# Performance work log

Measured on AMD Instinct MI355X. Metric: run time of the kernel, lower is better.

Reference implementation:

```python
import jax, jax.numpy as jnp
import numpy as np

EMBED = 2048
N_EXPERTS = 64
TOP_K = 8


def setup_inputs() -> dict:
    key = jax.random.key(0)
    k_x, k_w, k_b = jax.random.split(key, 3)
    inputs = jax.random.normal(k_x, (8, 4096, EMBED), dtype=jnp.float32)
    # nn.Linear(embed_size, num_experts): weight [E, D], bias [E]
    bound = 1.0 / np.sqrt(EMBED)
    W = jax.random.uniform(k_w, (N_EXPERTS, EMBED), dtype=jnp.float32, minval=-bound, maxval=bound)
    b = jax.random.uniform(k_b, (N_EXPERTS,), dtype=jnp.float32, minval=-bound, maxval=bound)
    return {"inputs": inputs, "W": W, "b": b}


def reference(inputs, W, b):
    # scores: [B, S, E]
    scores = jnp.einsum("bsd,ed->bse", inputs, W) + b
    topk_scores, indices = jax.lax.top_k(scores, TOP_K)  # [B,S,K]
    # scatter topk_scores into a zero mask (non-selected slots stay 0.0)
    onehot = jax.nn.one_hot(indices, N_EXPERTS, dtype=scores.dtype)  # [B,S,K,E]
    mask = jnp.einsum("bske,bsk->bse", onehot, topk_scores)
    router_output = jax.nn.softmax(mask, axis=-1)
    return (router_output, indices)
```

## Files before the change

kernel.cpp:

```cpp
#include <hip/hip_runtime.h>
#include <math.h>

#define N_TOKENS 32768
#define EMBED    2048
#define NEXP     64
#define TOPK     8
#define BM       64
#define BK       64
#define NCH      (EMBED / BK)
#define SCS      65
#define THRESH   1e-4f
#define WELEMS   (NEXP * EMBED)
#define FIXGRID  1024

typedef __attribute__((ext_vector_type(8)))  short short8;
typedef __attribute__((ext_vector_type(16))) float f32x16;
typedef __attribute__((ext_vector_type(4)))  unsigned int uint4v;

__device__ __forceinline__ unsigned pkbf(float a, float b) {
  unsigned r;
  asm("v_cvt_pk_bf16_f32 %0, %1, %2" : "=v"(r) : "v"(a), "v"(b));
  return r;
}

__device__ __forceinline__ void cvt8(float4 fa, float4 fb, short8* h8, short8* l8) {
  const unsigned h0 = pkbf(fa.x, fa.y), h1 = pkbf(fa.z, fa.w);
  const unsigned h2 = pkbf(fb.x, fb.y), h3 = pkbf(fb.z, fb.w);
  const float l0 = fa.x - __uint_as_float(h0 << 16);
  const float l1 = fa.y - __uint_as_float(h0 & 0xFFFF0000u);
  const float l2 = fa.z - __uint_as_float(h1 << 16);
  const float l3 = fa.w - __uint_as_float(h1 & 0xFFFF0000u);
  const float l4 = fb.x - __uint_as_float(h2 << 16);
  const float l5 = fb.y - __uint_as_float(h2 & 0xFFFF0000u);
  const float l6 = fb.z - __uint_as_float(h3 << 16);
  const float l7 = fb.w - __uint_as_float(h3 & 0xFFFF0000u);
  const uint4v H = {h0, h1, h2, h3};
  const uint4v L = {pkbf(l0, l1), pkbf(l2, l3), pkbf(l4, l5), pkbf(l6, l7)};
  *h8 = __builtin_bit_cast(short8, H);
  *l8 = __builtin_bit_cast(short8, L);
}

__global__ void split_w(const float* __restrict__ W, short* __restrict__ wh,
                        short* __restrict__ wl, int* __restrict__ gcnt) {
  if (blockIdx.x == 0 && threadIdx.x == 0) *gcnt = 0;
  const int T = blockIdx.x * 256 + threadIdx.x;
  const int n = T >> 8, kg8 = T & 255;
  const float4* W4 = (const float4*)W;
  float4 a = W4[n * 512 + kg8 * 2];
  float4 b = W4[n * 512 + kg8 * 2 + 1];
  short8 h, l;
  cvt8(a, b, &h, &l);
  *(short8*)&wh[(kg8 * 64 + n) * 8] = h;
  *(short8*)&wl[(kg8 * 64 + n) * 8] = l;
}

__global__ __launch_bounds__(256, 2)
void router_kernel(const float* __restrict__ x, const short* __restrict__ wh,
                   const short* __restrict__ wl, const float* __restrict__ bias,
                   int* __restrict__ gcnt, int* __restrict__ glist,
                   float* __restrict__ out) {
  __shared__ float4 lx[3][1024];
  float* sc = (float*)&lx[0][0];

  const int tid  = threadIdx.x;
  const int t0   = blockIdx.x * BM;
  const int lane = tid & 63;
  const int w    = tid >> 6;
  const int half = lane >> 5;
  const int r5   = lane & 31;
  const int tw   = (w & 1) * 32;
  const int ew   = (w >> 1) * 32;

  const float4* x4g = (const float4*)x;
  const short8* Bh  = (const short8*)wh;
  const short8* Bl  = (const short8*)wl;
  const int boff = half * 64 + ew + r5;

  const int row16 = tid >> 4;
  const int s4    = tid & 15;
  const int c4sw  = s4 ^ row16;
  const int wbase = (tid & 192);

  const float4* gbase = x4g + (size_t)(t0 + row16) * (EMBED / 4) + c4sw;

#pragma unroll
  for (int i = 0; i < 4; ++i)
    __builtin_amdgcn_global_load_lds((const void*)(gbase + (size_t)16 * i * (EMBED / 4)),
                                     (void*)&lx[0][i * 256 + wbase], 16, 0, 0);
#pragma unroll
  for (int i = 0; i < 4; ++i)
    __builtin_amdgcn_global_load_lds((const void*)(gbase + (size_t)16 * i * (EMBED / 4) + 16),
                                     (void*)&lx[1][i * 256 + wbase], 16, 0, 0);

  const int arow  = tw + r5;
  const int am    = arow & 15;
  const int abase = (arow >> 4) * 256 + am * 16;

  f32x16 acc;
#pragma unroll
  for (int i = 0; i < 16; ++i) acc[i] = 0.f;

  int bc = 0, bp = 2;
  for (int ch = 0; ch < NCH; ++ch) {
    if (ch + 1 < NCH) asm volatile("s_waitcnt vmcnt(4)" ::: "memory");
    else              asm volatile("s_waitcnt vmcnt(0)" ::: "memory");
    __builtin_amdgcn_s_barrier();
    __builtin_amdgcn_sched_barrier(0);

    short8 bh[4], bl[4];
#pragma unroll
    for (int s = 0; s < 4; ++s) {
      const int bi = (ch * 4 + s) * 128 + boff;
      bh[s] = Bh[bi]; bl[s] = Bl[bi];
    }
    __builtin_amdgcn_sched_barrier(0);

    if (ch + 2 < NCH) {
#pragma unroll
      for (int i = 0; i < 4; ++i)
        __builtin_amdgcn_global_load_lds(
            (const void*)(gbase + (size_t)16 * i * (EMBED / 4) + (ch + 2) * 16),
            (void*)&lx[bp][i * 256 + wbase], 16, 0, 0);
    }

#pragma unroll
    for (int s = 0; s < 4; ++s) {
      const int c0 = s * 4 + half * 2;
      float4 fa = lx[bc][abase + (c0 ^ am)];
      float4 fb = lx[bc][abase + ((c0 + 1) ^ am)];
      short8 ah, al;
      cvt8(fa, fb, &ah, &al);
      acc = __builtin_amdgcn_mfma_f32_32x32x16_bf16(ah, bh[s], acc, 0, 0, 0);
      acc = __builtin_amdgcn_mfma_f32_32x32x16_bf16(ah, bl[s], acc, 0, 0, 0);
      acc = __builtin_amdgcn_mfma_f32_32x32x16_bf16(al, bh[s], acc, 0, 0, 0);
    }
    bc = (bc == 2) ? 0 : bc + 1;
    bp = (bp == 2) ? 0 : bp + 1;
  }

  __syncthreads();

#pragma unroll
  for (int reg = 0; reg < 16; ++reg) {
    const int row = (reg & 3) + 8 * (reg >> 2) + 4 * half;
    sc[(tw + row) * SCS + ew + r5] = acc[reg];
  }
  __syncthreads();

  float* rout = out;
  float* iout = out + (size_t)N_TOKENS * NEXP;
  const float bias_l = bias[lane];

  for (int tb = 0; tb < 4; ++tb) {
    const int tbase = w * 16 + tb * 4;
    float orig[4]; unsigned cur[4];
#pragma unroll
    for (int i = 0; i < 4; ++i) {
      orig[i] = sc[(tbase + i) * SCS + lane] + bias_l;
      unsigned b = __float_as_uint(orig[i]);
      unsigned u = b ^ (((unsigned)((int)b >> 31)) | 0x80000000u);
      cur[i] = (u & 0xFFFFFFC0u) | (63u - (unsigned)lane);
    }
    float m[4], Z[4], ming[4], prev[4], morig[4];
    int myidx[4]; bool sel[4];
#pragma unroll
    for (int i = 0; i < 4; ++i) { sel[i] = false; morig[i] = 0.f; myidx[i] = 0; ming[i] = 1e30f; }

#pragma unroll
    for (int r = 0; r < 9; ++r) {
      unsigned v[4];
#pragma unroll
      for (int i = 0; i < 4; ++i) v[i] = cur[i];
#pragma unroll
      for (int s2 = 1; s2 < 64; s2 <<= 1) {
#pragma unroll
        for (int i = 0; i < 4; ++i) {
          unsigned o = (unsigned)__shfl_xor((int)v[i], s2);
          v[i] = v[i] > o ? v[i] : o;
        }
      }
#pragma unroll
      for (int i = 0; i < 4; ++i) {
        unsigned vb = (v[i] & 0x80000000u) ? (v[i] ^ 0x80000000u) : ~v[i];
        float fv = __uint_as_float(vb);
        if (r == 0) { m[i] = fmaxf(fv, 0.f); Z[i] = 56.f * expf(-m[i]) + expf(fv - m[i]); }
        else {
          ming[i] = fminf(ming[i], prev[i] - fv);
          if (r < 8) Z[i] += expf(fv - m[i]);
        }
        prev[i] = fv;
        if (r < 8) {
          if (lane == r) myidx[i] = 63 - (int)(v[i] & 63u);
          if (cur[i] == v[i]) { sel[i] = true; morig[i] = orig[i]; cur[i] = 0u; }
        }
      }
    }
#pragma unroll
    for (int i = 0; i < 4; ++i) {
      const int t = tbase + i;
      if (ming[i] < THRESH) {
        if (lane == 0) { int p = atomicAdd(gcnt, 1); glist[p] = t0 + t; }
      } else {
        const float p = expf(morig[i] - m[i]) / Z[i];
        rout[(size_t)(t0 + t) * NEXP + lane] = p;
        if (lane < TOPK) iout[(size_t)(t0 + t) * TOPK + lane] = (float)myidx[i];
      }
    }
  }
}

__global__ __launch_bounds__(256, 4)
void fixup_kernel(const float* __restrict__ x, const float* __restrict__ Wf,
                  const float* __restrict__ bias, const int* __restrict__ gcnt,
                  const int* __restrict__ glist, float* __restrict__ out) {
  __shared__ float4 xsh[512];
  __shared__ double sco[NEXP];
  const int tid  = threadIdx.x;
  const int lane = tid & 63;
  const int w    = tid >> 6;
  float* rout = out;
  float* iout = out + (size_t)N_TOKENS * NEXP;
  const int cnt = *gcnt;

  for (int j = blockIdx.x; j < cnt; j += FIXGRID) {
    const int tok = glist[j];
    const float4* xr = (const float4*)x + (size_t)tok * 512;
    xsh[tid] = xr[tid];
    xsh[tid + 256] = xr[tid + 256];
    __syncthreads();

    for (int i = 0; i < 16; ++i) {
      const int e = w * 16 + i;
      const float4* wr = (const float4*)Wf + (size_t)e * 512;
      double a = 0.0;
#pragma unroll
      for (int q = 0; q < 8; ++q) {
        float4 wv = wr[q * 64 + lane];
        float4 xv = xsh[q * 64 + lane];
        a = fma((double)xv.x, (double)wv.x, a);
        a = fma((double)xv.y, (double)wv.y, a);
        a = fma((double)xv.z, (double)wv.z, a);
        a = fma((double)xv.w, (double)wv.w, a);
      }
#pragma unroll
      for (int s2 = 1; s2 < 64; s2 <<= 1) a += __shfl_xor(a, s2);
      if (lane == 0) sco[e] = a + (double)bias[e];
    }
    __syncthreads();

    if (w == 0) {
      const double orig = sco[lane];
      double curd = orig, vals[8];
      int myidx = 0; double mym = 0.0;
#pragma unroll
      for (int r = 0; r < 8; ++r) {
        double v = curd; int id = lane;
#pragma unroll
        for (int s2 = 1; s2 < 64; s2 <<= 1) {
          const double ov = __shfl_xor(v, s2);
          const int    oi = __shfl_xor(id, s2);
          if (ov > v || (ov == v && oi < id)) { v = ov; id = oi; }
        }
        vals[r] = v;
        if (lane == r)  myidx = id;
        if (lane == id) { mym = orig; curd = -1e300; }
      }
      const double md = fmax(vals[0], 0.0);
      double Zd = 56.0 * exp(-md);
#pragma unroll
      for (int r = 0; r < 8; ++r) Zd += exp(vals[r] - md);
      const double p = exp(mym - md) / Zd;
      rout[(size_t)tok * NEXP + lane] = (float)p;
      if (lane < TOPK) iout[(size_t)tok * TOPK + lane] = (float)myidx;
    }
    __syncthreads();
  }
}

extern "C" void kernel_launch(void* const* d_in, const int* in_sizes, int n_in,
                              void* d_out, int out_size, void* d_ws, size_t ws_size,
                              hipStream_t stream) {
  const float* x = (const float*)d_in[0];
  const float* W = (const float*)d_in[1];
  const float* b = (const float*)d_in[2];
  short* wh = (short*)d_ws;
  short* wl = wh + WELEMS;
  int* gcnt  = (int*)(wl + WELEMS);
  int* glist = gcnt + 4;

  split_w<<<64, 256, 0, stream>>>(W, wh, wl, gcnt);
  router_kernel<<<N_TOKENS / BM, 256, 0, stream>>>(x, wh, wl, b, gcnt, glist,
                                                   (float*)d_out);
  fixup_kernel<<<FIXGRID, 256, 0, stream>>>(x, W, b, gcnt, glist, (float*)d_out);
}
```

Baseline: 465.9 us.

## Deepen x prefetch to four LDS buffers and software-pipeline weight loads

Moves from a 3-deep to a 4-deep LDS ring for x chunks, so x tiles are prefetched three chunks ahead instead of two. The global loads of the bf16 weight fragments for the next chunk are now issued a full iteration ahead into alternating register sets, so they overlap with the current chunk's MFMAs. The loop is unrolled by two and the last chunks are peeled, with explicit vmcnt waits. This adds LDS use, which may reduce occupancy, and more registers, and it relies on precise vmcnt accounting. It also removes an unused sel flag.

Measured after the change: 467.4 us. Within noise of the previous version (+0.3%).

```diff
diff --git a/kernel.cpp b/kernel.cpp
--- a/kernel.cpp
+++ b/kernel.cpp
@@ -59,7 +59,7 @@
                    const short* __restrict__ wl, const float* __restrict__ bias,
                    int* __restrict__ gcnt, int* __restrict__ glist,
                    float* __restrict__ out) {
-  __shared__ float4 lx[3][1024];
+  __shared__ float4 lx[4][1024];
   float* sc = (float*)&lx[0][0];
 
   const int tid  = threadIdx.x;
@@ -83,15 +83,6 @@
 
   const float4* gbase = x4g + (size_t)(t0 + row16) * (EMBED / 4) + c4sw;
 
-#pragma unroll
-  for (int i = 0; i < 4; ++i)
-    __builtin_amdgcn_global_load_lds((const void*)(gbase + (size_t)16 * i * (EMBED / 4)),
-                                     (void*)&lx[0][i * 256 + wbase], 16, 0, 0);
-#pragma unroll
-  for (int i = 0; i < 4; ++i)
-    __builtin_amdgcn_global_load_lds((const void*)(gbase + (size_t)16 * i * (EMBED / 4) + 16),
-                                     (void*)&lx[1][i * 256 + wbase], 16, 0, 0);
-
   const int arow  = tw + r5;
   const int am    = arow & 15;
   const int abase = (arow >> 4) * 256 + am * 16;
@@ -100,43 +91,90 @@
 #pragma unroll
   for (int i = 0; i < 16; ++i) acc[i] = 0.f;
 
-  int bc = 0, bp = 2;
-  for (int ch = 0; ch < NCH; ++ch) {
-    if (ch + 1 < NCH) asm volatile("s_waitcnt vmcnt(4)" ::: "memory");
-    else              asm volatile("s_waitcnt vmcnt(0)" ::: "memory");
-    __builtin_amdgcn_s_barrier();
-    __builtin_amdgcn_sched_barrier(0);
-
-    short8 bh[4], bl[4];
+  auto ISSUE_X = [&](int ch) {
+#pragma unroll
+    for (int i = 0; i < 4; ++i)
+      __builtin_amdgcn_global_load_lds(
+          (const void*)(gbase + (size_t)16 * i * (EMBED / 4) + ch * 16),
+          (void*)&lx[ch & 3][i * 256 + wbase], 16, 0, 0);
+  };
+  auto LOADB = [&](int ch, short8 (&bh)[4], short8 (&bl)[4]) {
 #pragma unroll
     for (int s = 0; s < 4; ++s) {
       const int bi = (ch * 4 + s) * 128 + boff;
       bh[s] = Bh[bi]; bl[s] = Bl[bi];
     }
-    __builtin_amdgcn_sched_barrier(0);
-
-    if (ch + 2 < NCH) {
-#pragma unroll
-      for (int i = 0; i < 4; ++i)
-        __builtin_amdgcn_global_load_lds(
-            (const void*)(gbase + (size_t)16 * i * (EMBED / 4) + (ch + 2) * 16),
-            (void*)&lx[bp][i * 256 + wbase], 16, 0, 0);
-    }
-
+  };
+  auto COMPUTE = [&](int ch, short8 (&bh)[4], short8 (&bl)[4]) {
 #pragma unroll
     for (int s = 0; s < 4; ++s) {
       const int c0 = s * 4 + half * 2;
-      float4 fa = lx[bc][abase + (c0 ^ am)];
-      float4 fb = lx[bc][abase + ((c0 + 1) ^ am)];
+      float4 fa = lx[ch & 3][abase + (c0 ^ am)];
+      float4 fb = lx[ch & 3][abase + ((c0 + 1) ^ am)];
       short8 ah, al;
       cvt8(fa, fb, &ah, &al);
       acc = __builtin_amdgcn_mfma_f32_32x32x16_bf16(ah, bh[s], acc, 0, 0, 0);
       acc = __builtin_amdgcn_mfma_f32_32x32x16_bf16(ah, bl[s], acc, 0, 0, 0);
       acc = __builtin_amdgcn_mfma_f32_32x32x16_bf16(al, bh[s], acc, 0, 0, 0);
     }
-    bc = (bc == 2) ? 0 : bc + 1;
-    bp = (bp == 2) ? 0 : bp + 1;
+  };
+
+  short8 bh0[4], bl0[4], bh1[4], bl1[4];
+
+  LOADB(0, bh0, bl0);
+  ISSUE_X(0); ISSUE_X(1); ISSUE_X(2);
+  asm volatile("s_waitcnt vmcnt(8)" ::: "memory");
+
+  for (int t = 0; t < 14; ++t) {
+    const int ch = 2 * t;
+    asm volatile("s_waitcnt vmcnt(24)" ::: "memory");
+    __builtin_amdgcn_s_barrier();
+    __builtin_amdgcn_sched_barrier(0);
+    LOADB(ch + 1, bh1, bl1);
+    __builtin_amdgcn_sched_barrier(0);
+    ISSUE_X(ch + 3);
+    __builtin_amdgcn_sched_barrier(0);
+    COMPUTE(ch, bh0, bl0);
+    __builtin_amdgcn_sched_barrier(0);
+    asm volatile("s_waitcnt vmcnt(16)" ::: "memory");
+    __builtin_amdgcn_s_barrier();
+    __builtin_amdgcn_sched_barrier(0);
+    LOADB(ch + 2, bh0, bl0);
+    __builtin_amdgcn_sched_barrier(0);
+    ISSUE_X(ch + 4);
+    __builtin_amdgcn_sched_barrier(0);
+    COMPUTE(ch + 1, bh1, bl1);
+    __builtin_amdgcn_sched_barrier(0);
   }
+
+  asm volatile("s_waitcnt vmcnt(24)" ::: "memory");
+  __builtin_amdgcn_s_barrier();
+  __builtin_amdgcn_sched_barrier(0);
+  LOADB(29, bh1, bl1);
+  __builtin_amdgcn_sched_barrier(0);
+  ISSUE_X(31);
+  __builtin_amdgcn_sched_barrier(0);
+  COMPUTE(28, bh0, bl0);
+  __builtin_amdgcn_sched_barrier(0);
+
+  asm volatile("s_waitcnt vmcnt(16)" ::: "memory");
+  __builtin_amdgcn_s_barrier();
+  __builtin_amdgcn_sched_barrier(0);
+  LOADB(30, bh0, bl0);
+  __builtin_amdgcn_sched_barrier(0);
+  COMPUTE(29, bh1, bl1);
+  __builtin_amdgcn_sched_barrier(0);
+
+  __builtin_amdgcn_s_barrier();
+  __builtin_amdgcn_sched_barrier(0);
+  LOADB(31, bh1, bl1);
+  __builtin_amdgcn_sched_barrier(0);
+  COMPUTE(30, bh0, bl0);
+  __builtin_amdgcn_sched_barrier(0);
+
+  __builtin_amdgcn_s_barrier();
+  __builtin_amdgcn_sched_barrier(0);
+  COMPUTE(31, bh1, bl1);
 
   __syncthreads();
 
@@ -162,9 +200,9 @@
       cur[i] = (u & 0xFFFFFFC0u) | (63u - (unsigned)lane);
     }
     float m[4], Z[4], ming[4], prev[4], morig[4];
-    int myidx[4]; bool sel[4];
-#pragma unroll
-    for (int i = 0; i < 4; ++i) { sel[i] = false; morig[i] = 0.f; myidx[i] = 0; ming[i] = 1e30f; }
+    int myidx[4];
+#pragma unroll
+    for (int i = 0; i < 4; ++i) { morig[i] = 0.f; myidx[i] = 0; ming[i] = 1e30f; }
 
 #pragma unroll
     for (int r = 0; r < 9; ++r) {
@@ -191,7 +229,7 @@
         prev[i] = fv;
         if (r < 8) {
           if (lane == r) myidx[i] = 63 - (int)(v[i] & 63u);
-          if (cur[i] == v[i]) { sel[i] = true; morig[i] = orig[i]; cur[i] = 0u; }
+          if (cur[i] == v[i]) { morig[i] = orig[i]; cur[i] = 0u; }
         }
       }
     }
```
